# Kernel optimization log

Measured on AMD Instinct MI355X. Metric: run time of the kernel, lower is better.

The kernel has to match this reference:

```python
import jax, jax.numpy as jnp
import numpy as np

N = 100000      # num nodes
E = 3200000     # num edges
R = 8           # num relations
C_IN, HID, C_OUT = 128, 64, 64


def rgcn_conv(x, W, root, bias, src, dst, etype):
    """One RGCNConv layer (PyG semantics, mean aggregation per relation).
    out[i] = bias + x[i] @ root + sum_r mean_{j in N_r(i)} x[j] @ W[r]
    """
    n = x.shape[0]
    # transform-then-gather: [R, N, H] avoids per-edge [E, C, H] matmuls
    xW = jnp.einsum('nc,rch->rnh', x, W)
    msg = xW[etype, src]                              # [E, H]
    # per-(relation, target-node) in-degree for mean normalization
    seg = etype * n + dst
    deg = jax.ops.segment_sum(jnp.ones((src.shape[0],), dtype=x.dtype), seg,
                              num_segments=R * n)      # [R*N]
    msg = msg / jnp.maximum(deg[seg], 1.0)[:, None]
    agg = jax.ops.segment_sum(msg, dst, num_segments=n)  # [N, H]
    return agg + x @ root + bias


def setup_inputs() -> dict:
    key = jax.random.key(0)
    ks = jax.random.split(key, 9)
    x = jax.random.normal(ks[0], (N, C_IN), dtype=jnp.float32)
    edge_index = jax.random.randint(ks[1], (2, E), 0, N)
    edge_type = jax.random.randint(ks[2], (E,), 0, R)
    s1 = 1.0 / np.sqrt(C_IN)
    s2 = 1.0 / np.sqrt(HID)
    W1 = jax.random.normal(ks[3], (R, C_IN, HID), dtype=jnp.float32) * s1
    root1 = jax.random.normal(ks[4], (C_IN, HID), dtype=jnp.float32) * s1
    b1 = jnp.zeros((HID,), dtype=jnp.float32)
    W2 = jax.random.normal(ks[5], (R, HID, C_OUT), dtype=jnp.float32) * s2
    root2 = jax.random.normal(ks[6], (HID, C_OUT), dtype=jnp.float32) * s2
    b2 = jnp.zeros((C_OUT,), dtype=jnp.float32)
    return {"x": x, "edge_index": edge_index, "edge_type": edge_type,
            "W1": W1, "root1": root1, "b1": b1,
            "W2": W2, "root2": root2, "b2": b2}


def reference(x, edge_index, edge_type, W1, root1, b1, W2, root2, b2):
    src, dst = edge_index[0], edge_index[1]
    h = rgcn_conv(x, W1, root1, b1, src, dst, edge_type)
    h = jax.nn.relu(h)  # dropout p=0.0 is identity
    out = rgcn_conv(h, W2, root2, b2, src, dst, edge_type)
    return out
```

## Files before the change

kernel.cpp:

```cpp
#include <hip/hip_runtime.h>

#define N_NODES 100000
#define N_EDGES 3200000
#define R_REL   8
#define C_IN    128
#define HID     64
#define WCOLS   576

#define NBUCK 500
#define NPB   200
#define NBLK  256
#define CHUNK 12500
#define NCELL (NBUCK * NBLK)
#define BCAP  7680

typedef __attribute__((ext_vector_type(8))) short  short8;
typedef __attribute__((ext_vector_type(4))) float  float4v;

__device__ __forceinline__ float bf2f(unsigned short u) {
    union { unsigned int i; float f; } v; v.i = ((unsigned int)u) << 16; return v.f;
}
__device__ __forceinline__ unsigned short f2bf(float f) {
    union { float f; unsigned int i; } v; v.f = f;
    unsigned int r = v.i + 0x7FFFu + ((v.i >> 16) & 1u);
    return (unsigned short)(r >> 16);
}
__device__ __forceinline__ float rl_f(float v, int j) {
    union { float f; int i; } a, b; a.f = v;
    b.i = __builtin_amdgcn_readlane(a.i, j);
    return b.f;
}

__global__ void prep_wcat(const float* __restrict__ W1,
                          const float* __restrict__ root1,
                          const float* __restrict__ W2,
                          const float* __restrict__ root2,
                          unsigned short* __restrict__ BT1,
                          unsigned short* __restrict__ BT2) {
    int idx = blockIdx.x * 256 + threadIdx.x;
    const int T1 = WCOLS * C_IN;
    const int T2 = WCOLS * HID;
    if (idx < T1) {
        int c = idx / C_IN, k = idx % C_IN;
        float v;
        if (c < 512) { int r = c >> 6, h = c & 63; v = W1[r * (C_IN * 64) + k * 64 + h]; }
        else         { v = root1[k * 64 + (c - 512)]; }
        BT1[idx] = f2bf(v);
    } else if (idx < T1 + T2) {
        int j = idx - T1;
        int c = j / HID, k = j % HID;
        float v;
        if (c < 512) { int r = c >> 6, h = c & 63; v = W2[r * (HID * 64) + k * 64 + h]; }
        else         { v = root2[k * 64 + (c - 512)]; }
        BT2[j] = f2bf(v);
    }
}

__global__ __launch_bounds__(1024)
void edge_sort_local(const int* __restrict__ src, const int* __restrict__ dst,
                     const int* __restrict__ et,
                     unsigned int* __restrict__ esort,
                     int* __restrict__ bcountT, int* __restrict__ lstartT) {
    __shared__ int cnt[NBUCK], cur[NBUCK], tsum[1024];
    __shared__ unsigned int sedge[CHUNK];
    const int blk = blockIdx.x, tid = threadIdx.x;
    const int e0 = blk * CHUNK;

    for (int i = tid; i < NBUCK; i += 1024) cnt[i] = 0;
    __syncthreads();
    for (int i = tid; i < CHUNK; i += 1024)
        atomicAdd(&cnt[dst[e0 + i] / NPB], 1);
    __syncthreads();

    int v = (tid < NBUCK) ? cnt[tid] : 0;
    tsum[tid] = v; __syncthreads();
    for (int off = 1; off < 1024; off <<= 1) {
        int t = (tid >= off) ? tsum[tid - off] : 0;
        __syncthreads(); tsum[tid] += t; __syncthreads();
    }
    if (tid < NBUCK) cur[tid] = tsum[tid] - v;
    __syncthreads();

    for (int b = tid; b < NBUCK; b += 1024) {
        bcountT[blk * NBUCK + b] = cnt[b];
        lstartT[blk * NBUCK + b] = cur[b];
    }
    __syncthreads();

    for (int i = tid; i < CHUNK; i += 1024) {
        int d = dst[e0 + i];
        int b = d / NPB;
        int pos = atomicAdd(&cur[b], 1);
        sedge[pos] = ((unsigned int)src[e0 + i] << 11) |
                     ((unsigned int)(d - b * NPB) << 3) | (unsigned int)et[e0 + i];
    }
    __syncthreads();
    for (int i = tid; i < CHUNK; i += 1024) esort[e0 + i] = sedge[i];
}

__global__ __launch_bounds__(1024)
void bucket_build(const unsigned int* __restrict__ esort,
                  const int* __restrict__ bcountT, const int* __restrict__ lstartT,
                  unsigned int* __restrict__ elist,
                  int* __restrict__ rowstart8) {
    __shared__ int   cnt[2048], cur[2048], tsum[1024];
    __shared__ int   rpos[NBLK], rloff[NBLK];
    __shared__ unsigned int sedge[BCAP];
    __shared__ unsigned int selist[BCAP];

    const int b = blockIdx.x, tid = threadIdx.x;

    for (int i = tid; i < 2048; i += 1024) cnt[i] = 0;
    int myrl = 0, myls = 0;
    if (tid < NBLK) {
        myrl = bcountT[tid * NBUCK + b];
        myls = lstartT[tid * NBUCK + b];
        rpos[tid] = tid * CHUNK + myls;
    }
    __syncthreads();

    tsum[tid] = myrl; __syncthreads();
    for (int off = 1; off < 1024; off <<= 1) {
        int t = (tid >= off) ? tsum[tid - off] : 0;
        __syncthreads(); tsum[tid] += t; __syncthreads();
    }
    const int total = tsum[NBLK - 1];
    if (tid < NBLK) rloff[tid] = tsum[tid] - myrl;
    __syncthreads();

    tsum[tid] = myls; __syncthreads();
    for (int off = 512; off > 0; off >>= 1) {
        if (tid < off) tsum[tid] += tsum[tid + off];
        __syncthreads();
    }
    const int seg0 = tsum[0];
    __syncthreads();
    const bool fits = (total <= BCAP);

    for (int i = tid; i < total; i += 1024) {
        int lo = 0, hi = NBLK - 1;
        while (lo < hi) { int mid = (lo + hi + 1) >> 1; if (rloff[mid] <= i) lo = mid; else hi = mid - 1; }
        unsigned int e = esort[rpos[lo] + (i - rloff[lo])];
        if (fits) sedge[i] = e;
        atomicAdd(&cnt[(int)((e >> 3) & 255u) * 8 + (int)(e & 7u)], 1);
    }
    __syncthreads();

    int base = tid * 2;
    int c0 = cnt[base], c1 = cnt[base + 1];
    int s = c0 + c1;
    tsum[tid] = s; __syncthreads();
    for (int off = 1; off < 1024; off <<= 1) {
        int t = (tid >= off) ? tsum[tid - off] : 0;
        __syncthreads(); tsum[tid] += t; __syncthreads();
    }
    int texcl = tsum[tid] - s;
    cur[base] = texcl; cur[base + 1] = texcl + c0;
    __syncthreads();

    for (int i = tid; i < NPB * 8; i += 1024)
        rowstart8[(b * NPB) * 8 + i] = seg0 + cur[i];
    if (b == NBUCK - 1 && tid == 0) rowstart8[N_NODES * 8] = N_EDGES;
    __syncthreads();

    for (int i = tid; i < total; i += 1024) {
        unsigned int e;
        if (fits) e = sedge[i];
        else {
            int lo = 0, hi = NBLK - 1;
            while (lo < hi) { int mid = (lo + hi + 1) >> 1; if (rloff[mid] <= i) lo = mid; else hi = mid - 1; }
            e = esort[rpos[lo] + (i - rloff[lo])];
        }
        int r = (int)(e & 7u);
        int j = (int)((e >> 3) & 255u) * 8 + r;
        int p = atomicAdd(&cur[j], 1);
        unsigned int eo = (e >> 11) * WCOLS + (unsigned int)(r * 64);
        if (fits) selist[p] = eo;
        else      elist[seg0 + p] = eo;
    }
    __syncthreads();

    if (fits) {
        for (int i = tid; i < total; i += 1024)
            elist[seg0 + i] = selist[i];
    }
}

__global__ __launch_bounds__(512)
void gemm_l1(const float* __restrict__ A,
             const unsigned short* __restrict__ BT,
             unsigned short* __restrict__ Out, int nrows) {
    constexpr int K = C_IN;
    constexpr int LDB = K + 8;
    __shared__ __align__(16) unsigned short Blds[2][64 * LDB];
    __shared__ __align__(16) unsigned short stage[8][16 * 64];

    const int wave = threadIdx.x >> 6, lane = threadIdx.x & 63;
    const int l15 = lane & 15, quad = lane >> 4;
    const int rowbase = blockIdx.x * 128 + wave * 16;
    int arow = rowbase + l15;
    if (arow >= nrows) arow = nrows - 1;

    short8 afrag[4];
#pragma unroll
    for (int ks = 0; ks < 4; ++ks) {
        const float* p = A + (size_t)arow * K + ks * 32 + quad * 8;
        float4v u0 = *(const float4v*)p;
        float4v u1 = *(const float4v*)(p + 4);
        short8 f;
        f[0] = (short)f2bf(u0[0]); f[1] = (short)f2bf(u0[1]);
        f[2] = (short)f2bf(u0[2]); f[3] = (short)f2bf(u0[3]);
        f[4] = (short)f2bf(u1[0]); f[5] = (short)f2bf(u1[1]);
        f[6] = (short)f2bf(u1[2]); f[7] = (short)f2bf(u1[3]);
        afrag[ks] = f;
    }

    for (int i = threadIdx.x; i < 1024; i += 512) {
        int r = i >> 4, c = (i & 15) * 8;
        *(uint4*)&Blds[0][r * LDB + c] = *(const uint4*)(BT + r * K + c);
    }
    __syncthreads();

    int cur = 0;
    for (int chunk = 0; chunk < 9; ++chunk) {
        uint4 p0, p1;
        const int i0 = threadIdx.x, i1 = threadIdx.x + 512;
        if (chunk < 8) {
            const unsigned short* src = BT + (size_t)(chunk + 1) * 64 * K;
            p0 = *(const uint4*)(src + (i0 >> 4) * K + (i0 & 15) * 8);
            p1 = *(const uint4*)(src + (i1 >> 4) * K + (i1 & 15) * 8);
        }

        float4v acc[4];
#pragma unroll
        for (int ct = 0; ct < 4; ++ct) { acc[ct][0] = 0.f; acc[ct][1] = 0.f; acc[ct][2] = 0.f; acc[ct][3] = 0.f; }
#pragma unroll
        for (int ct = 0; ct < 4; ++ct)
#pragma unroll
            for (int ks = 0; ks < 4; ++ks) {
                short8 bfrag = *(const short8*)(&Blds[cur][(ct * 16 + l15) * LDB + ks * 32 + quad * 8]);
                acc[ct] = __builtin_amdgcn_mfma_f32_16x16x32_bf16(afrag[ks], bfrag, acc[ct], 0, 0, 0);
            }

#pragma unroll
        for (int ct = 0; ct < 4; ++ct)
#pragma unroll
            for (int r = 0; r < 4; ++r)
                stage[wave][(quad * 4 + r) * 64 + ct * 16 + l15] = f2bf(acc[ct][r]);
        {
            int r = lane >> 2, j = lane & 3;
            int orow = rowbase + r;
            if (orow < nrows) {
#pragma unroll
                for (int p = 0; p < 2; ++p) {
                    int c0 = (j + p * 4) * 8;
                    uint4 v = *(const uint4*)&stage[wave][r * 64 + c0];
                    *(uint4*)(Out + (size_t)orow * WCOLS + chunk * 64 + c0) = v;
                }
            }
        }

        if (chunk < 8) {
            *(uint4*)&Blds[cur ^ 1][(i0 >> 4) * LDB + (i0 & 15) * 8] = p0;
            *(uint4*)&Blds[cur ^ 1][(i1 >> 4) * LDB + (i1 & 15) * 8] = p1;
            cur ^= 1;
        }
        __syncthreads();
    }
}

__global__ __launch_bounds__(512)
void gemm_l2(const unsigned short* __restrict__ A,
             const unsigned short* __restrict__ BT,
             unsigned short* __restrict__ Out, int nrows) {
    constexpr int K = HID;
    constexpr int LDB = K + 8;
    __shared__ __align__(16) unsigned short Blds[WCOLS * LDB];
    __shared__ __align__(16) unsigned short stage[8][16 * 64];

    const int wave = threadIdx.x >> 6, lane = threadIdx.x & 63;
    const int l15 = lane & 15, quad = lane >> 4;

    for (int i = threadIdx.x; i < WCOLS * K / 8; i += 512) {
        int c = i >> 3, kv = (i & 7) * 8;
        *(uint4*)&Blds[c * LDB + kv] = *(const uint4*)(BT + c * K + kv);
    }
    __syncthreads();

    const int ntiles = (nrows + 127) / 128;
    for (int t = blockIdx.x; t < ntiles; t += gridDim.x) {
        const int rowbase = t * 128 + wave * 16;
        int arow = rowbase + l15;
        if (arow >= nrows) arow = nrows - 1;
        short8 afrag[2];
#pragma unroll
        for (int ks = 0; ks < 2; ++ks)
            afrag[ks] = *(const short8*)(A + (size_t)arow * K + ks * 32 + quad * 8);

        for (int chunk = 0; chunk < 9; ++chunk) {
            float4v acc[4];
#pragma unroll
            for (int ct = 0; ct < 4; ++ct) { acc[ct][0] = 0.f; acc[ct][1] = 0.f; acc[ct][2] = 0.f; acc[ct][3] = 0.f; }
#pragma unroll
            for (int ct = 0; ct < 4; ++ct)
#pragma unroll
                for (int ks = 0; ks < 2; ++ks) {
                    short8 bfrag = *(const short8*)(&Blds[(chunk * 64 + ct * 16 + l15) * LDB + ks * 32 + quad * 8]);
                    acc[ct] = __builtin_amdgcn_mfma_f32_16x16x32_bf16(afrag[ks], bfrag, acc[ct], 0, 0, 0);
                }

#pragma unroll
            for (int ct = 0; ct < 4; ++ct)
#pragma unroll
                for (int r = 0; r < 4; ++r)
                    stage[wave][(quad * 4 + r) * 64 + ct * 16 + l15] = f2bf(acc[ct][r]);
            {
                int r = lane >> 2, j = lane & 3;
                int orow = rowbase + r;
                if (orow < nrows) {
#pragma unroll
                    for (int p = 0; p < 2; ++p) {
                        int c0 = (j + p * 4) * 8;
                        uint4 v = *(const uint4*)&stage[wave][r * 64 + c0];
                        *(uint4*)(Out + (size_t)orow * WCOLS + chunk * 64 + c0) = v;
                    }
                }
            }
        }
    }
}

template <int MODE>
__global__ __launch_bounds__(256)
void agg_fused(const unsigned short* __restrict__ XW,
               const unsigned int* __restrict__ elist,
               const int* __restrict__ rowstart8,
               const float* __restrict__ bias,
               void* __restrict__ outp) {
    const int wave = threadIdx.x >> 6, lane = threadIdx.x & 63;
    const int n = blockIdx.x * 4 + wave;
    int r9 = 0;
    if (lane < 9) r9 = rowstart8[n * 8 + lane];
    const int b0 = __builtin_amdgcn_readlane(r9, 0);
    const int b1 = __builtin_amdgcn_readlane(r9, 1);
    const int b2 = __builtin_amdgcn_readlane(r9, 2);
    const int b3 = __builtin_amdgcn_readlane(r9, 3);
    const int b4 = __builtin_amdgcn_readlane(r9, 4);
    const int b5 = __builtin_amdgcn_readlane(r9, 5);
    const int b6 = __builtin_amdgcn_readlane(r9, 6);
    const int b7 = __builtin_amdgcn_readlane(r9, 7);
    const int b8 = __builtin_amdgcn_readlane(r9, 8);
    const int beg = b0, end = b8;

    auto invlen = [](int a, int bnd) {
        int l = bnd - a; return 1.0f / (float)(l > 1 ? l : 1);
    };
    const float il0 = invlen(b0, b1), il1 = invlen(b1, b2);
    const float il2 = invlen(b2, b3), il3 = invlen(b3, b4);
    const float il4 = invlen(b4, b5), il5 = invlen(b5, b6);
    const float il6 = invlen(b6, b7), il7 = invlen(b7, b8);

    const unsigned short* XWl = XW + lane;

    float acc = 0.f;
    int i = beg;
    while (i < end) {
        int m = end - i; if (m > 64) m = 64;
        int idx = i + lane; if (idx >= end) idx = end - 1;
        unsigned int ub = elist[idx];
        float wb = il0;
        wb = (idx >= b1) ? il1 : wb;
        wb = (idx >= b2) ? il2 : wb;
        wb = (idx >= b3) ? il3 : wb;
        wb = (idx >= b4) ? il4 : wb;
        wb = (idx >= b5) ? il5 : wb;
        wb = (idx >= b6) ? il6 : wb;
        wb = (idx >= b7) ? il7 : wb;

        int j = 0;
        for (; j + 16 <= m; j += 16) {
            float vv[16], ww[16];
#pragma unroll
            for (int t = 0; t < 16; ++t) {
                unsigned int u = (unsigned int)__builtin_amdgcn_readlane((int)ub, j + t);
                ww[t] = rl_f(wb, j + t);
                vv[t] = bf2f(XWl[u]);
            }
#pragma unroll
            for (int t = 0; t < 16; ++t) acc += ww[t] * vv[t];
        }
        for (; j + 4 <= m; j += 4) {
            float vv[4], ww[4];
#pragma unroll
            for (int t = 0; t < 4; ++t) {
                unsigned int u = (unsigned int)__builtin_amdgcn_readlane((int)ub, j + t);
                ww[t] = rl_f(wb, j + t);
                vv[t] = bf2f(XWl[u]);
            }
#pragma unroll
            for (int t = 0; t < 4; ++t) acc += ww[t] * vv[t];
        }
        for (; j < m; ++j) {
            unsigned int u = (unsigned int)__builtin_amdgcn_readlane((int)ub, j);
            float w = rl_f(wb, j);
            acc += w * bf2f(XWl[u]);
        }
        i += m;
    }

    float res = acc + bf2f(XW[(size_t)n * WCOLS + 512 + lane]) + bias[lane];
    if (MODE == 0) {
        res = res > 0.f ? res : 0.f;
        ((unsigned short*)outp)[(size_t)n * 64 + lane] = f2bf(res);
    } else {
        ((float*)outp)[(size_t)n * 64 + lane] = res;
    }
}

extern "C" void kernel_launch(void* const* d_in, const int* in_sizes, int n_in,
                              void* d_out, int out_size, void* d_ws, size_t ws_size,
                              hipStream_t stream) {
    const float* x     = (const float*)d_in[0];
    const int*   eidx  = (const int*)d_in[1];
    const int*   etyp  = (const int*)d_in[2];
    const float* W1    = (const float*)d_in[3];
    const float* root1 = (const float*)d_in[4];
    const float* b1    = (const float*)d_in[5];
    const float* W2    = (const float*)d_in[6];
    const float* root2 = (const float*)d_in[7];
    const float* b2    = (const float*)d_in[8];
    float*       out   = (float*)d_out;

    char* ws = (char*)d_ws;
    size_t off = 0;
    auto alloc = [&](size_t bytes) { char* p = ws + off; off += (bytes + 255) & ~(size_t)255; return p; };

    unsigned short* xW       = (unsigned short*)alloc((size_t)N_NODES * WCOLS * 2);
    unsigned short* h        = (unsigned short*)alloc((size_t)N_NODES * HID * 2);
    unsigned int*   elist    = (unsigned int*)alloc((size_t)N_EDGES * 4);
    int*            rowstart8= (int*)alloc(((size_t)N_NODES * 8 + 1) * 4);
    unsigned short* BT1      = (unsigned short*)alloc((size_t)WCOLS * C_IN * 2);
    unsigned short* BT2      = (unsigned short*)alloc((size_t)WCOLS * HID * 2);

    unsigned int* esort   = (unsigned int*)xW;
    int*          bcountT = (int*)((char*)xW + (size_t)N_EDGES * 4);
    int*          lstartT = bcountT + NCELL;

    const int* srcp = eidx;
    const int* dstp = eidx + N_EDGES;

    prep_wcat<<<(WCOLS * (C_IN + HID) + 255) / 256, 256, 0, stream>>>(W1, root1, W2, root2, BT1, BT2);

    edge_sort_local<<<NBLK, 1024, 0, stream>>>(srcp, dstp, etyp, esort, bcountT, lstartT);
    bucket_build<<<NBUCK, 1024, 0, stream>>>(esort, bcountT, lstartT, elist, rowstart8);

    const int gemm1_grid = (N_NODES + 127) / 128;
    const int agg_grid   = N_NODES / 4;

    gemm_l1<<<gemm1_grid, 512, 0, stream>>>(x, BT1, xW, N_NODES);
    agg_fused<0><<<agg_grid, 256, 0, stream>>>(xW, elist, rowstart8, b1, (void*)h);

    gemm_l2<<<256, 512, 0, stream>>>(h, BT2, xW, N_NODES);
    agg_fused<1><<<agg_grid, 256, 0, stream>>>(xW, elist, rowstart8, b2, (void*)out);
}
```

Measured before the change: 379.0 us.

## Fuse weight prep into edge sort, use shuffle scans, per-run bucket reads

Folds the weight-transpose prep kernel into edge_sort_local (256 blocks × 432 threads covers all 110592 elements), which removes one launch. Replaces the barrier-heavy Hillis-Steele shared-memory scans with a wave-shuffle two-level exclusive scan. In bucket_build, the per-element binary search over run offsets is replaced by four threads per run reading contiguous segments. BCAP is lowered slightly to make room for the extra shared arrays, so slightly fewer buckets take the in-LDS path.

```diff
diff --git a/kernel.cpp b/kernel.cpp
--- a/kernel.cpp
+++ b/kernel.cpp
@@ -12,7 +12,8 @@
 #define NBLK  256
 #define CHUNK 12500
 #define NCELL (NBUCK * NBLK)
-#define BCAP  7680
+#define BCAP  7424
+#define PREPC 432
 
 typedef __attribute__((ext_vector_type(8))) short  short8;
 typedef __attribute__((ext_vector_type(4))) float  float4v;
@@ -31,41 +32,64 @@
     return b.f;
 }
 
-__global__ void prep_wcat(const float* __restrict__ W1,
-                          const float* __restrict__ root1,
-                          const float* __restrict__ W2,
-                          const float* __restrict__ root2,
-                          unsigned short* __restrict__ BT1,
-                          unsigned short* __restrict__ BT2) {
-    int idx = blockIdx.x * 256 + threadIdx.x;
-    const int T1 = WCOLS * C_IN;
-    const int T2 = WCOLS * HID;
-    if (idx < T1) {
-        int c = idx / C_IN, k = idx % C_IN;
-        float v;
-        if (c < 512) { int r = c >> 6, h = c & 63; v = W1[r * (C_IN * 64) + k * 64 + h]; }
-        else         { v = root1[k * 64 + (c - 512)]; }
-        BT1[idx] = f2bf(v);
-    } else if (idx < T1 + T2) {
-        int j = idx - T1;
-        int c = j / HID, k = j % HID;
-        float v;
-        if (c < 512) { int r = c >> 6, h = c & 63; v = W2[r * (HID * 64) + k * 64 + h]; }
-        else         { v = root2[k * 64 + (c - 512)]; }
-        BT2[j] = f2bf(v);
-    }
+__device__ __forceinline__ int block_exscan_1024(int v, int tid, int* wsum, int* tot) {
+    __syncthreads();
+    const int lane = tid & 63, wid = tid >> 6;
+    int s = v;
+#pragma unroll
+    for (int d = 1; d < 64; d <<= 1) {
+        int t = __shfl_up(s, d, 64);
+        if (lane >= d) s += t;
+    }
+    if (lane == 63) wsum[wid] = s;
+    __syncthreads();
+    if (wid == 0) {
+        int ws = (lane < 16) ? wsum[lane] : 0;
+#pragma unroll
+        for (int d = 1; d < 16; d <<= 1) {
+            int t = __shfl_up(ws, d, 64);
+            if (lane >= d) ws += t;
+        }
+        if (lane < 16) wsum[lane] = ws;
+    }
+    __syncthreads();
+    int wexcl = (wid == 0) ? 0 : wsum[wid - 1];
+    if (tot) *tot = wsum[15];
+    return wexcl + s - v;
 }
 
 __global__ __launch_bounds__(1024)
 void edge_sort_local(const int* __restrict__ src, const int* __restrict__ dst,
                      const int* __restrict__ et,
+                     const float* __restrict__ W1, const float* __restrict__ root1,
+                     const float* __restrict__ W2, const float* __restrict__ root2,
+                     unsigned short* __restrict__ BT1, unsigned short* __restrict__ BT2,
                      unsigned int* __restrict__ esort,
                      int* __restrict__ bcountT, int* __restrict__ lstartT) {
-    __shared__ int cnt[NBUCK], cur[NBUCK], tsum[1024];
+    __shared__ int cnt[NBUCK], cur[NBUCK], wsum[16];
     __shared__ unsigned int sedge[CHUNK];
     const int blk = blockIdx.x, tid = threadIdx.x;
     const int e0 = blk * CHUNK;
 
+    if (tid < PREPC) {
+        int idx = blk * PREPC + tid;
+        const int T1 = WCOLS * C_IN;
+        if (idx < T1) {
+            int c = idx / C_IN, k = idx % C_IN;
+            float v;
+            if (c < 512) { int r = c >> 6, h = c & 63; v = W1[r * (C_IN * 64) + k * 64 + h]; }
+            else         { v = root1[k * 64 + (c - 512)]; }
+            BT1[idx] = f2bf(v);
+        } else {
+            int j = idx - T1;
+            int c = j / HID, k = j % HID;
+            float v;
+            if (c < 512) { int r = c >> 6, h = c & 63; v = W2[r * (HID * 64) + k * 64 + h]; }
+            else         { v = root2[k * 64 + (c - 512)]; }
+            BT2[j] = f2bf(v);
+        }
+    }
+
     for (int i = tid; i < NBUCK; i += 1024) cnt[i] = 0;
     __syncthreads();
     for (int i = tid; i < CHUNK; i += 1024)
@@ -73,17 +97,11 @@
     __syncthreads();
 
     int v = (tid < NBUCK) ? cnt[tid] : 0;
-    tsum[tid] = v; __syncthreads();
-    for (int off = 1; off < 1024; off <<= 1) {
-        int t = (tid >= off) ? tsum[tid - off] : 0;
-        __syncthreads(); tsum[tid] += t; __syncthreads();
-    }
-    if (tid < NBUCK) cur[tid] = tsum[tid] - v;
-    __syncthreads();
-
-    for (int b = tid; b < NBUCK; b += 1024) {
-        bcountT[blk * NBUCK + b] = cnt[b];
-        lstartT[blk * NBUCK + b] = cur[b];
+    int ex = block_exscan_1024(v, tid, wsum, nullptr);
+    if (tid < NBUCK) {
+        cur[tid] = ex;
+        bcountT[blk * NBUCK + tid] = v;
+        lstartT[blk * NBUCK + tid] = ex;
     }
     __syncthreads();
 
@@ -103,8 +121,8 @@
                   const int* __restrict__ bcountT, const int* __restrict__ lstartT,
                   unsigned int* __restrict__ elist,
                   int* __restrict__ rowstart8) {
-    __shared__ int   cnt[2048], cur[2048], tsum[1024];
-    __shared__ int   rpos[NBLK], rloff[NBLK];
+    __shared__ int   cnt[2048], cur[2048];
+    __shared__ int   rlen_s[NBLK], rpos[NBLK], rloff[NBLK], wsum[16];
     __shared__ unsigned int sedge[BCAP];
     __shared__ unsigned int selist[BCAP];
 
@@ -115,47 +133,34 @@
     if (tid < NBLK) {
         myrl = bcountT[tid * NBUCK + b];
         myls = lstartT[tid * NBUCK + b];
+        rlen_s[tid] = myrl;
         rpos[tid] = tid * CHUNK + myls;
     }
-    __syncthreads();
-
-    tsum[tid] = myrl; __syncthreads();
-    for (int off = 1; off < 1024; off <<= 1) {
-        int t = (tid >= off) ? tsum[tid - off] : 0;
-        __syncthreads(); tsum[tid] += t; __syncthreads();
-    }
-    const int total = tsum[NBLK - 1];
-    if (tid < NBLK) rloff[tid] = tsum[tid] - myrl;
-    __syncthreads();
-
-    tsum[tid] = myls; __syncthreads();
-    for (int off = 512; off > 0; off >>= 1) {
-        if (tid < off) tsum[tid] += tsum[tid + off];
-        __syncthreads();
-    }
-    const int seg0 = tsum[0];
+
+    int total;
+    int rex = block_exscan_1024(myrl, tid, wsum, &total);
+    if (tid < NBLK) rloff[tid] = rex;
+
+    int seg0;
+    (void)block_exscan_1024(myls, tid, wsum, &seg0);
     __syncthreads();
     const bool fits = (total <= BCAP);
 
-    for (int i = tid; i < total; i += 1024) {
-        int lo = 0, hi = NBLK - 1;
-        while (lo < hi) { int mid = (lo + hi + 1) >> 1; if (rloff[mid] <= i) lo = mid; else hi = mid - 1; }
-        unsigned int e = esort[rpos[lo] + (i - rloff[lo])];
-        if (fits) sedge[i] = e;
-        atomicAdd(&cnt[(int)((e >> 3) & 255u) * 8 + (int)(e & 7u)], 1);
+    {
+        const int run = tid >> 2, sub = tid & 3;
+        const int len = rlen_s[run], lp = rpos[run], ro = rloff[run];
+        for (int k = sub; k < len; k += 4) {
+            unsigned int e = esort[lp + k];
+            if (fits) sedge[ro + k] = e;
+            atomicAdd(&cnt[(int)((e >> 3) & 255u) * 8 + (int)(e & 7u)], 1);
+        }
     }
     __syncthreads();
 
     int base = tid * 2;
     int c0 = cnt[base], c1 = cnt[base + 1];
-    int s = c0 + c1;
-    tsum[tid] = s; __syncthreads();
-    for (int off = 1; off < 1024; off <<= 1) {
-        int t = (tid >= off) ? tsum[tid - off] : 0;
-        __syncthreads(); tsum[tid] += t; __syncthreads();
-    }
-    int texcl = tsum[tid] - s;
-    cur[base] = texcl; cur[base + 1] = texcl + c0;
+    int ex2 = block_exscan_1024(c0 + c1, tid, wsum, nullptr);
+    cur[base] = ex2; cur[base + 1] = ex2 + c0;
     __syncthreads();
 
     for (int i = tid; i < NPB * 8; i += 1024)
@@ -163,26 +168,27 @@
     if (b == NBUCK - 1 && tid == 0) rowstart8[N_NODES * 8] = N_EDGES;
     __syncthreads();
 
-    for (int i = tid; i < total; i += 1024) {
-        unsigned int e;
-        if (fits) e = sedge[i];
-        else {
-            int lo = 0, hi = NBLK - 1;
-            while (lo < hi) { int mid = (lo + hi + 1) >> 1; if (rloff[mid] <= i) lo = mid; else hi = mid - 1; }
-            e = esort[rpos[lo] + (i - rloff[lo])];
-        }
-        int r = (int)(e & 7u);
-        int j = (int)((e >> 3) & 255u) * 8 + r;
-        int p = atomicAdd(&cur[j], 1);
-        unsigned int eo = (e >> 11) * WCOLS + (unsigned int)(r * 64);
-        if (fits) selist[p] = eo;
-        else      elist[seg0 + p] = eo;
-    }
-    __syncthreads();
-
     if (fits) {
+        for (int i = tid; i < total; i += 1024) {
+            unsigned int e = sedge[i];
+            int r = (int)(e & 7u);
+            int j = (int)((e >> 3) & 255u) * 8 + r;
+            int p = atomicAdd(&cur[j], 1);
+            selist[p] = (e >> 11) * WCOLS + (unsigned int)(r * 64);
+        }
+        __syncthreads();
         for (int i = tid; i < total; i += 1024)
             elist[seg0 + i] = selist[i];
+    } else {
+        const int run = tid >> 2, sub = tid & 3;
+        const int len = rlen_s[run], lp = rpos[run];
+        for (int k = sub; k < len; k += 4) {
+            unsigned int e = esort[lp + k];
+            int r = (int)(e & 7u);
+            int j = (int)((e >> 3) & 255u) * 8 + r;
+            int p = atomicAdd(&cur[j], 1);
+            elist[seg0 + p] = (e >> 11) * WCOLS + (unsigned int)(r * 64);
+        }
     }
 }
 
@@ -449,9 +455,9 @@
     const int* srcp = eidx;
     const int* dstp = eidx + N_EDGES;
 
-    prep_wcat<<<(WCOLS * (C_IN + HID) + 255) / 256, 256, 0, stream>>>(W1, root1, W2, root2, BT1, BT2);
-
-    edge_sort_local<<<NBLK, 1024, 0, stream>>>(srcp, dstp, etyp, esort, bcountT, lstartT);
+    edge_sort_local<<<NBLK, 1024, 0, stream>>>(srcp, dstp, etyp,
+                                               W1, root1, W2, root2, BT1, BT2,
+                                               esort, bcountT, lstartT);
     bucket_build<<<NBUCK, 1024, 0, stream>>>(esort, bcountT, lstartT, elist, rowstart8);
 
     const int gemm1_grid = (N_NODES + 127) / 128;
```

New measurement: 367.0 us. -3.2%, faster.
